# Performance work log

Measured on AMD Instinct MI355X. Metric: run time of the kernel, lower is better.

Reference implementation:

```python
import math
import jax, jax.numpy as jnp
import numpy as np

H, KV, D = 16, 4, 128          # num_heads, num_kv_heads, head_dim
HID = 2048                      # hidden_size
ROPE_BASE = 1e6
EPS = 1e-6


def setup_inputs() -> dict:
    key = jax.random.key(0)
    ks = jax.random.split(key, 3)
    B, S = 2, 2048
    s = 0.02
    return {
        "x": jax.random.normal(ks[0], (B, S, HID), jnp.float32),
        "w_qkv": jax.random.normal(ks[1], (2 * H * D + 2 * KV * D, HID), jnp.float32) * s,
        "w_o": jax.random.normal(ks[2], (HID, H * D), jnp.float32) * s,
        "q_norm_w": jnp.ones((D,), jnp.float32),
        "q_norm_b": jnp.zeros((D,), jnp.float32),
        "k_norm_w": jnp.ones((D,), jnp.float32),
        "k_norm_b": jnp.zeros((D,), jnp.float32),
    }


def _layernorm(x, w, b):
    mu = jnp.mean(x, axis=-1, keepdims=True)
    xc = x - mu
    var = jnp.mean(xc * xc, axis=-1, keepdims=True)
    return xc * jax.lax.rsqrt(var + EPS) * w + b


def _rope(x, cos, sin):
    # x: [B, h, S, D]; cos/sin: [S, D/2]; interleaved real/imag pairs
    xr, xi = x[..., 0::2], x[..., 1::2]
    c, s = cos[None, None], sin[None, None]
    out = jnp.stack([xr * c - xi * s, xr * s + xi * c], axis=-1)
    return out.reshape(x.shape)


def reference(x, w_qkv, w_o, q_norm_w, q_norm_b, k_norm_w, k_norm_b):
    B, S, _ = x.shape
    qkv = x @ w_qkv.T                                  # [B,S,2*H*D+2*KV*D]
    qg, k, v = jnp.split(qkv, [2 * H * D, 2 * H * D + KV * D], axis=-1)
    q, gate = jnp.split(qg, 2, axis=-1)                # [B,S,H*D] each

    q = q.reshape(B, S, H, D).transpose(0, 2, 1, 3)    # [B,H,S,D]
    k = k.reshape(B, S, KV, D).transpose(0, 2, 1, 3)   # [B,KV,S,D]
    v = v.reshape(B, S, KV, D).transpose(0, 2, 1, 3)

    q = _layernorm(q, q_norm_w, q_norm_b)
    k = _layernorm(k, k_norm_w, k_norm_b)

    inv = 1.0 / (ROPE_BASE ** (jnp.arange(0, D, 2, dtype=jnp.float32) / D))
    freqs = jnp.outer(jnp.arange(S, dtype=jnp.float32), inv)  # [S, D/2]
    cos, sin = jnp.cos(freqs), jnp.sin(freqs)
    q = _rope(q, cos, sin)
    k = _rope(k, cos, sin)

    rep = H // KV
    k = jnp.repeat(k, rep, axis=1)                     # [B,H,S,D]
    v = jnp.repeat(v, rep, axis=1)

    scores = jnp.einsum('bhqd,bhkd->bhqk', q, k) / math.sqrt(D)
    causal = jnp.tril(jnp.ones((S, S), bool))
    scores = jnp.where(causal[None, None], scores, -jnp.inf)
    attn = jax.nn.softmax(scores, axis=-1)
    out = jnp.einsum('bhqk,bhkd->bhqd', attn, v)
    out = out.transpose(0, 2, 1, 3).reshape(B, S, H * D)
    out = out * jax.nn.sigmoid(gate)
    return out @ w_o.T
```

## Files before the change

kernel.cpp:

```cpp
#include <hip/hip_runtime.h>
#include <hip/hip_bf16.h>

typedef __bf16 bf16_t;
typedef __bf16 bf16x2 __attribute__((ext_vector_type(2)));
typedef __bf16 bf16x4v __attribute__((ext_vector_type(4)));
typedef __bf16 bf16x8 __attribute__((ext_vector_type(8)));
typedef float f32x4 __attribute__((ext_vector_type(4)));

#define LOG2E 1.4426950408889634f
#define QSCALE (0.08838834764831843f * 1.4426950408889634f)

__global__ __launch_bounds__(256) void cvt_all(const float* __restrict__ x, bf16_t* __restrict__ xb,
                                               const float* __restrict__ wq, bf16_t* __restrict__ wqb,
                                               const float* __restrict__ wo, bf16_t* __restrict__ wob) {
  int i = blockIdx.x * 256 + threadIdx.x;
  const float* in; bf16_t* out; int idx;
  if (i < 2097152)      { in = x;  out = xb;  idx = i; }
  else if (i < 4718592) { in = wq; out = wqb; idx = i - 2097152; }
  else                  { in = wo; out = wob; idx = i - 4718592; }
  float4 v = ((const float4*)in)[idx];
  bf16x4v o;
  o[0] = (__bf16)v.x; o[1] = (__bf16)v.y; o[2] = (__bf16)v.z; o[3] = (__bf16)v.w;
  *(bf16x4v*)(out + (size_t)idx * 4) = o;
}

__global__ __launch_bounds__(256) void rope_tables(float* __restrict__ cosT,
                                                   float* __restrict__ sinT) {
  int idx = blockIdx.x * 256 + threadIdx.x;
  int s = idx >> 6, i = idx & 63;
  float inv = __builtin_amdgcn_exp2f(-(float)i * (19.931568569324174f / 64.0f));
  float f = (float)s * inv;
  cosT[idx] = cosf(f);
  sinT[idx] = sinf(f);
}

template<int MI, int NI, typename OT>
__global__ __launch_bounds__(512) void gemm8p(const bf16_t* __restrict__ A,
                                              const bf16_t* __restrict__ B,
                                              OT* __restrict__ C,
                                              int M, int N, int K) {
  constexpr int BM = MI * 32;
  constexpr int BN = NI * 64;
  constexpr int NA = BM / 64;
  constexpr int NB = BN / 64;
  constexpr int ST = NA + NB;

  __shared__ bf16_t LA[2][BM * 64];
  __shared__ bf16_t LB[2][BN * 64];

  int nb = N / BN;
  int cpx = gridDim.x >> 3;
  int bid = blockIdx.x;
  int swz = (bid & 7) * cpx + (bid >> 3);
  int bm = swz / nb, bn = swz % nb;
  int m0 = bm * BM, n0 = bn * BN;
  int tid = threadIdx.x, lane = tid & 63, wv = tid >> 6;
  int wr = wv >> 2, wc = wv & 3, lr = lane & 15, g = lane >> 4;
  int T = K >> 6;

  auto stageI = [&](int kt, int bi, int s) {
    int k0 = kt << 6;
    if (s < NA) {
      int c = s * 512 + tid;
      int row = c >> 3, lc = (c & 7) ^ (row & 7);
      __builtin_amdgcn_global_load_lds(
          (const __attribute__((address_space(1))) void*)(A + (size_t)(m0 + row) * K + k0 + lc * 8),
          (__attribute__((address_space(3))) void*)&LA[bi][(s * 512 + wv * 64) * 8], 16, 0, 0);
    } else {
      int c = (s - NA) * 512 + tid;
      int row = c >> 3, lc = (c & 7) ^ (row & 7);
      __builtin_amdgcn_global_load_lds(
          (const __attribute__((address_space(1))) void*)(B + (size_t)(n0 + row) * K + k0 + lc * 8),
          (__attribute__((address_space(3))) void*)&LB[bi][((s - NA) * 512 + wv * 64) * 8], 16, 0, 0);
    }
  };

  f32x4 acc[MI][NI];
#pragma unroll
  for (int i = 0; i < MI; i++)
#pragma unroll
    for (int j = 0; j < NI; j++)
#pragma unroll
      for (int r = 0; r < 4; r++) acc[i][j][r] = 0.f;

#pragma unroll
  for (int s = 0; s < ST; s++) stageI(0, 0, s);
  asm volatile("s_waitcnt vmcnt(0)" ::: "memory");
  __builtin_amdgcn_s_barrier();
  asm volatile("" ::: "memory");

  int ofk0 = ((0 + g) ^ (lr & 7)) << 3;
  int ofk1 = ((4 + g) ^ (lr & 7)) << 3;
  int offA = (wr * (MI * 16) + lr) * 64;
  int offB = (wc * (NI * 16) + lr) * 64;

  for (int t = 0; t < T; t++) {
    int bi = t & 1, bo = bi ^ 1;
    const bf16_t* la = LA[bi];
    const bf16_t* lb = LB[bi];
    bool pre = (t + 1 < T);
    if (pre) {
#pragma unroll
      for (int s = 0; s < ST; s++) stageI(t + 1, bo, s);
    }

    bf16x8 bq0[NI], bq1[NI];
#pragma unroll
    for (int ni = 0; ni < NI; ni++) bq0[ni] = *(const bf16x8*)&lb[offB + ni * 1024 + ofk0];
#pragma unroll
    for (int ni = 0; ni < NI; ni++) bq1[ni] = *(const bf16x8*)&lb[offB + ni * 1024 + ofk1];
#pragma unroll
    for (int q = 0; q < MI / 4; q++) {
      bf16x8 af0[4], af1[4];
#pragma unroll
      for (int i = 0; i < 4; i++)
        af0[i] = *(const bf16x8*)&la[offA + (q * 4 + i) * 1024 + ofk0];
#pragma unroll
      for (int i = 0; i < 4; i++)
#pragma unroll
        for (int ni = 0; ni < NI; ni++)
          acc[q * 4 + i][ni] =
              __builtin_amdgcn_mfma_f32_16x16x32_bf16(af0[i], bq0[ni], acc[q * 4 + i][ni], 0, 0, 0);
#pragma unroll
      for (int i = 0; i < 4; i++)
        af1[i] = *(const bf16x8*)&la[offA + (q * 4 + i) * 1024 + ofk1];
#pragma unroll
      for (int i = 0; i < 4; i++)
#pragma unroll
        for (int ni = 0; ni < NI; ni++)
          acc[q * 4 + i][ni] =
              __builtin_amdgcn_mfma_f32_16x16x32_bf16(af1[i], bq1[ni], acc[q * 4 + i][ni], 0, 0, 0);
    }

    if (pre) {
      asm volatile("s_waitcnt vmcnt(0) lgkmcnt(0)" ::: "memory");
      __builtin_amdgcn_s_barrier();
      asm volatile("" ::: "memory");
    }
  }

#pragma unroll
  for (int mi = 0; mi < MI; mi++)
#pragma unroll
    for (int ni = 0; ni < NI; ni++) {
      int m = m0 + wr * (MI * 16) + mi * 16 + g * 4;
      int n = n0 + wc * (NI * 16) + ni * 16 + lr;
#pragma unroll
      for (int r = 0; r < 4; r++) C[(size_t)(m + r) * N + n] = (OT)acc[mi][ni][r];
    }
}

__global__ __launch_bounds__(256) void ln_rope(const bf16_t* __restrict__ qkv,
                                               const float* __restrict__ qw, const float* __restrict__ qb,
                                               const float* __restrict__ kw, const float* __restrict__ kb,
                                               const float* __restrict__ cosT, const float* __restrict__ sinT,
                                               bf16_t* __restrict__ Qr, bf16_t* __restrict__ Kr) {
  int row = blockIdx.x;
  int b = row >> 11, s = row & 2047;
  int tid = threadIdx.x, gi = tid >> 4, li = tid & 15;
  const bf16_t* base = qkv + (size_t)row * 5120;
  float4 c4 = *(const float4*)(cosT + (s << 6) + (li << 2));
  float4 s4 = *(const float4*)(sinT + (s << 6) + (li << 2));
#pragma unroll
  for (int it = 0; it < 2; it++) {
    int head;
    if (it == 0) head = gi;
    else { if (gi >= 4) break; head = 16 + gi; }
    bool isq = (it == 0);
    int off = isq ? (head << 7) : (4096 + ((head - 16) << 7));
    bf16x8 xv = *(const bf16x8*)(base + off + (li << 3));
    float xf[8];
#pragma unroll
    for (int j = 0; j < 8; j++) xf[j] = (float)xv[j];
    float sum = 0.f;
#pragma unroll
    for (int j = 0; j < 8; j++) sum += xf[j];
#pragma unroll
    for (int m = 1; m < 16; m <<= 1) sum += __shfl_xor(sum, m);
    float mu = sum * 0.0078125f;
    float vs = 0.f;
#pragma unroll
    for (int j = 0; j < 8; j++) { xf[j] -= mu; vs += xf[j] * xf[j]; }
#pragma unroll
    for (int m = 1; m < 16; m <<= 1) vs += __shfl_xor(vs, m);
    float rs = rsqrtf(vs * 0.0078125f + 1e-6f);
    const float* w = isq ? qw : kw;
    const float* bb = isq ? qb : kb;
    float4 w0 = *(const float4*)(w + (li << 3));
    float4 w1 = *(const float4*)(w + (li << 3) + 4);
    float4 b0 = *(const float4*)(bb + (li << 3));
    float4 b1 = *(const float4*)(bb + (li << 3) + 4);
    float y[8];
    y[0] = xf[0] * rs * w0.x + b0.x; y[1] = xf[1] * rs * w0.y + b0.y;
    y[2] = xf[2] * rs * w0.z + b0.z; y[3] = xf[3] * rs * w0.w + b0.w;
    y[4] = xf[4] * rs * w1.x + b1.x; y[5] = xf[5] * rs * w1.y + b1.y;
    y[6] = xf[6] * rs * w1.z + b1.z; y[7] = xf[7] * rs * w1.w + b1.w;
    float cc[4] = { c4.x, c4.y, c4.z, c4.w };
    float ss[4] = { s4.x, s4.y, s4.z, s4.w };
    bf16x8 ov;
#pragma unroll
    for (int p = 0; p < 4; p++) {
      float o0 = y[2 * p] * cc[p] - y[2 * p + 1] * ss[p];
      float o1 = y[2 * p] * ss[p] + y[2 * p + 1] * cc[p];
      if (isq) { o0 *= QSCALE; o1 *= QSCALE; }
      ov[2 * p] = (__bf16)o0; ov[2 * p + 1] = (__bf16)o1;
    }
    size_t dst = isq ? ((((size_t)(b * 16 + head)) * 2048 + s) * 128 + (li << 3))
                     : ((((size_t)(b * 4 + (head - 16))) * 2048 + s) * 128 + (li << 3));
    *(bf16x8*)((isq ? Qr : Kr) + dst) = ov;
  }
}

__global__ __launch_bounds__(256) void vtrans(const bf16_t* __restrict__ qkv,
                                              bf16_t* __restrict__ Vt) {
  int bid = blockIdx.x;
  int sb = bid & 63, kv = (bid >> 6) & 3, b = bid >> 8;
  int s0 = sb << 5;
  __shared__ bf16_t T[128 * 33];
  int tid = threadIdx.x;
#pragma unroll
  for (int i = 0; i < 16; i++) {
    int idx = i * 256 + tid;
    int r = idx >> 7, d = idx & 127;
    T[d * 33 + r] = qkv[((size_t)(b * 2048 + s0 + r)) * 5120 + 4608 + (kv << 7) + d];
  }
  __syncthreads();
#pragma unroll
  for (int j = 0; j < 16; j++) {
    int idx = j * 256 + tid;
    int d = idx >> 5, sc = idx & 31;
    Vt[(((size_t)(b * 4 + kv)) * 128 + d) * 2048 + s0 + sc] = T[d * 33 + sc];
  }
}

__global__ __launch_bounds__(256, 3) void attn(const bf16_t* __restrict__ Qr,
                                               const bf16_t* __restrict__ Kr,
                                               const bf16_t* __restrict__ Vt,
                                               const bf16_t* __restrict__ qkv,
                                               bf16_t* __restrict__ ag) {
  __shared__ bf16_t Ks[2][32 * 128];
  __shared__ bf16_t Vs[2][128 * 32];
  int bid = blockIdx.x;
  int hb = bid & 31;
  int h = hb & 15, b = hb >> 4;
  int pr = bid >> 5;
  int kvh = h >> 2;
  int tid = threadIdx.x, lane = tid & 63, wv = tid >> 6;
  int lr = lane & 15, g = lane >> 4;
  int r0base = ((lr >> 2) << 3) + (lr & 3);

  const bf16_t* Kg = Kr + ((size_t)(b * 4 + kvh)) * 2048 * 128;
  const bf16_t* Vg = Vt + ((size_t)(b * 4 + kvh)) * 128 * 2048;

  auto stage = [&](int buf, int kv0) {
#pragma unroll
    for (int i = 0; i < 2; i++) {
      int c = i * 256 + tid;
      int row = c >> 4, lc = (c & 15) ^ (row & 15);
      __builtin_amdgcn_global_load_lds(
          (const __attribute__((address_space(1))) void*)(Kg + (size_t)(kv0 + row) * 128 + lc * 8),
          (__attribute__((address_space(3))) void*)&Ks[buf][c * 8], 16, 0, 0);
    }
#pragma unroll
    for (int i = 0; i < 2; i++) {
      int c = i * 256 + tid;
      int d = c >> 2, cv = (c & 3) ^ ((d >> 1) & 3);
      __builtin_amdgcn_global_load_lds(
          (const __attribute__((address_space(1))) void*)(Vg + (size_t)d * 2048 + kv0 + cv * 8),
          (__attribute__((address_space(3))) void*)&Vs[buf][c * 8], 16, 0, 0);
    }
  };

  auto sm = [&](const f32x4& s0, const f32x4& s1, int qrow, int kvabs, bool dia,
                float& mrun, float& lsp, bf16x8& pb, f32x4 (&oac)[8]) {
    float tt[8];
#pragma unroll
    for (int r = 0; r < 4; r++) { tt[r] = s0[r]; tt[4 + r] = s1[r]; }
    if (dia) {
#pragma unroll
      for (int r = 0; r < 4; r++) {
        if (kvabs + r > qrow)     tt[r]     = -1e30f;
        if (kvabs + 4 + r > qrow) tt[4 + r] = -1e30f;
      }
    }
    float lm = fmaxf(fmaxf(fmaxf(tt[0], tt[1]), tt[2]),
                     fmaxf(fmaxf(tt[3], tt[4]), fmaxf(fmaxf(tt[5], tt[6]), tt[7])));
    if (__all(lm <= mrun + 8.f)) {
      float ps = 0.f;
#pragma unroll
      for (int i = 0; i < 8; i++) {
        float pv = __builtin_amdgcn_exp2f(tt[i] - mrun);
        pb[i] = (__bf16)pv; ps += pv;
      }
      lsp += ps;
    } else {
      float pm = lm;
      pm = fmaxf(pm, __shfl_xor(pm, 16));
      pm = fmaxf(pm, __shfl_xor(pm, 32));
      float mnew = fmaxf(mrun, pm);
      float corr = __builtin_amdgcn_exp2f(mrun - mnew);
      float ps = 0.f;
#pragma unroll
      for (int i = 0; i < 8; i++) {
        float pv = __builtin_amdgcn_exp2f(tt[i] - mnew);
        pb[i] = (__bf16)pv; ps += pv;
      }
      lsp = lsp * corr + ps;
      mrun = mnew;
#pragma unroll
      for (int dt = 0; dt < 8; dt++)
#pragma unroll
        for (int r = 0; r < 4; r++) oac[dt][r] *= corr;
    }
  };

  for (int phase = 0; phase < 2; phase++) {
    int qb = phase ? (31 - pr) : pr;
    int qw0 = qb << 6;
    int qw = qw0 + (wv << 4);
    int qrow = qw + lr;
    int qmax = qw + 15;
    int nt = (qb + 1) << 1;

    const bf16_t* Qg = Qr + (((size_t)(b * 16 + h)) * 2048 + qrow) * 128;
    bf16x8 qf[4];
#pragma unroll
    for (int ds = 0; ds < 4; ds++) qf[ds] = *(const bf16x8*)(Qg + ds * 32 + g * 8);

    f32x4 oa[8];
#pragma unroll
    for (int i = 0; i < 8; i++)
#pragma unroll
      for (int r = 0; r < 4; r++) oa[i][r] = 0.f;
    float mrun = -1e30f, lsp = 0.f;

    stage(0, 0);
    asm volatile("s_waitcnt vmcnt(0)" ::: "memory");
    __builtin_amdgcn_s_barrier();
    asm volatile("" ::: "memory");
    for (int t = 0; t < nt; t++) {
      int cur = t & 1;
      if (t + 1 < nt) stage(cur ^ 1, (t + 1) << 5);
      int kvb = t << 5;
      if (kvb <= qmax) {
        const bf16_t* kb = Ks[cur];
        const bf16_t* vb = Vs[cur];
        int ra = r0base, rb2 = r0base + 4;
        bf16x8 a0[4], a1[4];
#pragma unroll
        for (int ds = 0; ds < 4; ds++) {
          a0[ds] = *(const bf16x8*)&kb[ra * 128 + (((ds * 4 + g) ^ (ra & 15)) << 3)];
          a1[ds] = *(const bf16x8*)&kb[rb2 * 128 + (((ds * 4 + g) ^ (rb2 & 15)) << 3)];
        }
        f32x4 s0, s1;
#pragma unroll
        for (int r = 0; r < 4; r++) { s0[r] = 0.f; s1[r] = 0.f; }
        __builtin_amdgcn_s_setprio(1);
#pragma unroll
        for (int ds = 0; ds < 4; ds++) {
          s0 = __builtin_amdgcn_mfma_f32_16x16x32_bf16(a0[ds], qf[ds], s0, 0, 0, 0);
          s1 = __builtin_amdgcn_mfma_f32_16x16x32_bf16(a1[ds], qf[ds], s1, 0, 0, 0);
        }
        __builtin_amdgcn_s_setprio(0);
        int kvabs = kvb + (g << 3);
        bool dia = (kvb + 31 > qw);
        bf16x8 pb;
        sm(s0, s1, qrow, kvabs, dia, mrun, lsp, pb, oa);
        __builtin_amdgcn_s_setprio(1);
#pragma unroll
        for (int dt = 0; dt < 8; dt++) {
          int d = dt * 16 + lr;
          bf16x8 va = *(const bf16x8*)&vb[d * 32 + ((g ^ ((d >> 1) & 3)) << 3)];
          oa[dt] = __builtin_amdgcn_mfma_f32_16x16x32_bf16(va, pb, oa[dt], 0, 0, 0);
        }
        __builtin_amdgcn_s_setprio(0);
      }
      asm volatile("s_waitcnt vmcnt(0) lgkmcnt(0)" ::: "memory");
      __builtin_amdgcn_s_barrier();
      asm volatile("" ::: "memory");
    }

    float ls = lsp + __shfl_xor(lsp, 16);
    ls += __shfl_xor(ls, 32);
    float invl = __builtin_amdgcn_rcpf(ls);

    size_t ob = ((size_t)b * 2048 + qrow) * 2048 + (h << 7);
    size_t gb = ((size_t)b * 2048 + qrow) * 5120 + 2048 + (h << 7);
#pragma unroll
    for (int dt = 0; dt < 8; dt++) {
      int d = dt * 16 + (g << 2);
      bf16x4v gt = *(const bf16x4v*)(qkv + gb + d);
      bf16x4v o;
      o[0] = (__bf16)(oa[dt][0] * invl * __builtin_amdgcn_rcpf(1.f + __builtin_amdgcn_exp2f(-(float)gt[0] * LOG2E)));
      o[1] = (__bf16)(oa[dt][1] * invl * __builtin_amdgcn_rcpf(1.f + __builtin_amdgcn_exp2f(-(float)gt[1] * LOG2E)));
      o[2] = (__bf16)(oa[dt][2] * invl * __builtin_amdgcn_rcpf(1.f + __builtin_amdgcn_exp2f(-(float)gt[2] * LOG2E)));
      o[3] = (__bf16)(oa[dt][3] * invl * __builtin_amdgcn_rcpf(1.f + __builtin_amdgcn_exp2f(-(float)gt[3] * LOG2E)));
      *(bf16x4v*)(ag + ob + d) = o;
    }
  }
}

extern "C" void kernel_launch(void* const* d_in, const int* in_sizes, int n_in,
                              void* d_out, int out_size, void* d_ws, size_t ws_size,
                              hipStream_t stream) {
  const float* x    = (const float*)d_in[0];
  const float* wqkv = (const float*)d_in[1];
  const float* wo   = (const float*)d_in[2];
  const float* qnw  = (const float*)d_in[3];
  const float* qnb  = (const float*)d_in[4];
  const float* knw  = (const float*)d_in[5];
  const float* knb  = (const float*)d_in[6];
  float* out = (float*)d_out;

  char* p = (char*)d_ws;
  bf16_t* xb  = (bf16_t*)p;
  bf16_t* ag  = xb;
  p += (size_t)16777216;
  bf16_t* wqb = (bf16_t*)p;
  bf16_t* Qr  = wqb;
  p += (size_t)20971520;
  bf16_t* wob = (bf16_t*)p; p += (size_t)8388608;
  bf16_t* qkv = (bf16_t*)p; p += (size_t)41943040;
  bf16_t* Kr  = (bf16_t*)p; p += (size_t)4194304;
  bf16_t* Vt  = (bf16_t*)p; p += (size_t)4194304;
  float* cosT = (float*)p;  p += (size_t)524288;
  float* sinT = (float*)p;  p += (size_t)524288;

  cvt_all<<<22528, 256, 0, stream>>>(x, xb, wqkv, wqb, wo, wob);
  rope_tables<<<512, 256, 0, stream>>>(cosT, sinT);

  gemm8p<8, 5, bf16_t><<<256, 512, 0, stream>>>(xb, wqb, qkv, 4096, 5120, 2048);

  ln_rope<<<4096, 256, 0, stream>>>(qkv, qnw, qnb, knw, knb, cosT, sinT, Qr, Kr);
  vtrans<<<512, 256, 0, stream>>>(qkv, Vt);

  attn<<<512, 256, 0, stream>>>(Qr, Kr, Vt, qkv, ag);

  gemm8p<4, 4, float><<<256, 512, 0, stream>>>(ag, wob, out, 4096, 2048, 2048);
}
```

Measured before the change: 232.7 us.

## Shrink GEMM K-tile to 32 and use smaller 128-row tiles for higher occupancy

Result: slower. 282.4 us (+21.4%).

```diff
diff --git a/kernel.cpp b/kernel.cpp
--- a/kernel.cpp
+++ b/kernel.cpp
@@ -34,19 +34,19 @@
   sinT[idx] = sinf(f);
 }
 
-template<int MI, int NI, typename OT>
-__global__ __launch_bounds__(512) void gemm8p(const bf16_t* __restrict__ A,
-                                              const bf16_t* __restrict__ B,
-                                              OT* __restrict__ C,
-                                              int M, int N, int K) {
-  constexpr int BM = MI * 32;
+template<int NI, typename OT>
+__global__ __launch_bounds__(512, 4) void gemmk(const bf16_t* __restrict__ A,
+                                                const bf16_t* __restrict__ B,
+                                                OT* __restrict__ C,
+                                                int M, int N, int K) {
+  constexpr int BM = 128;
   constexpr int BN = NI * 64;
-  constexpr int NA = BM / 64;
-  constexpr int NB = BN / 64;
+  constexpr int NA = 1;
+  constexpr int NB = BN / 128;
   constexpr int ST = NA + NB;
 
-  __shared__ bf16_t LA[2][BM * 64];
-  __shared__ bf16_t LB[2][BN * 64];
+  __shared__ bf16_t LA[2][BM * 32];
+  __shared__ bf16_t LB[2][BN * 32];
 
   int nb = N / BN;
   int cpx = gridDim.x >> 3;
@@ -56,28 +56,28 @@
   int m0 = bm * BM, n0 = bn * BN;
   int tid = threadIdx.x, lane = tid & 63, wv = tid >> 6;
   int wr = wv >> 2, wc = wv & 3, lr = lane & 15, g = lane >> 4;
-  int T = K >> 6;
+  int T = K >> 5;
 
   auto stageI = [&](int kt, int bi, int s) {
-    int k0 = kt << 6;
+    int k0 = kt << 5;
     if (s < NA) {
-      int c = s * 512 + tid;
-      int row = c >> 3, lc = (c & 7) ^ (row & 7);
+      int c = tid;
+      int row = c >> 2, lc = (c & 3) ^ (row & 3);
       __builtin_amdgcn_global_load_lds(
           (const __attribute__((address_space(1))) void*)(A + (size_t)(m0 + row) * K + k0 + lc * 8),
-          (__attribute__((address_space(3))) void*)&LA[bi][(s * 512 + wv * 64) * 8], 16, 0, 0);
+          (__attribute__((address_space(3))) void*)&LA[bi][wv * 512], 16, 0, 0);
     } else {
       int c = (s - NA) * 512 + tid;
-      int row = c >> 3, lc = (c & 7) ^ (row & 7);
+      int row = c >> 2, lc = (c & 3) ^ (row & 3);
       __builtin_amdgcn_global_load_lds(
           (const __attribute__((address_space(1))) void*)(B + (size_t)(n0 + row) * K + k0 + lc * 8),
           (__attribute__((address_space(3))) void*)&LB[bi][((s - NA) * 512 + wv * 64) * 8], 16, 0, 0);
     }
   };
 
-  f32x4 acc[MI][NI];
-#pragma unroll
-  for (int i = 0; i < MI; i++)
+  f32x4 acc[4][NI];
+#pragma unroll
+  for (int i = 0; i < 4; i++)
 #pragma unroll
     for (int j = 0; j < NI; j++)
 #pragma unroll
@@ -89,10 +89,9 @@
   __builtin_amdgcn_s_barrier();
   asm volatile("" ::: "memory");
 
-  int ofk0 = ((0 + g) ^ (lr & 7)) << 3;
-  int ofk1 = ((4 + g) ^ (lr & 7)) << 3;
-  int offA = (wr * (MI * 16) + lr) * 64;
-  int offB = (wc * (NI * 16) + lr) * 64;
+  int ofk = (g ^ (lr & 3)) << 3;
+  int offA = (wr * 64 + lr) * 32;
+  int offB = (wc * (NI * 16) + lr) * 32;
 
   for (int t = 0; t < T; t++) {
     int bi = t & 1, bo = bi ^ 1;
@@ -104,33 +103,16 @@
       for (int s = 0; s < ST; s++) stageI(t + 1, bo, s);
     }
 
-    bf16x8 bq0[NI], bq1[NI];
-#pragma unroll
-    for (int ni = 0; ni < NI; ni++) bq0[ni] = *(const bf16x8*)&lb[offB + ni * 1024 + ofk0];
-#pragma unroll
-    for (int ni = 0; ni < NI; ni++) bq1[ni] = *(const bf16x8*)&lb[offB + ni * 1024 + ofk1];
-#pragma unroll
-    for (int q = 0; q < MI / 4; q++) {
-      bf16x8 af0[4], af1[4];
-#pragma unroll
-      for (int i = 0; i < 4; i++)
-        af0[i] = *(const bf16x8*)&la[offA + (q * 4 + i) * 1024 + ofk0];
-#pragma unroll
-      for (int i = 0; i < 4; i++)
-#pragma unroll
-        for (int ni = 0; ni < NI; ni++)
-          acc[q * 4 + i][ni] =
-              __builtin_amdgcn_mfma_f32_16x16x32_bf16(af0[i], bq0[ni], acc[q * 4 + i][ni], 0, 0, 0);
-#pragma unroll
-      for (int i = 0; i < 4; i++)
-        af1[i] = *(const bf16x8*)&la[offA + (q * 4 + i) * 1024 + ofk1];
-#pragma unroll
-      for (int i = 0; i < 4; i++)
-#pragma unroll
-        for (int ni = 0; ni < NI; ni++)
-          acc[q * 4 + i][ni] =
-              __builtin_amdgcn_mfma_f32_16x16x32_bf16(af1[i], bq1[ni], acc[q * 4 + i][ni], 0, 0, 0);
-    }
+    bf16x8 bq[NI], af[4];
+#pragma unroll
+    for (int ni = 0; ni < NI; ni++) bq[ni] = *(const bf16x8*)&lb[offB + ni * 512 + ofk];
+#pragma unroll
+    for (int i = 0; i < 4; i++)     af[i]  = *(const bf16x8*)&la[offA + i * 512 + ofk];
+#pragma unroll
+    for (int i = 0; i < 4; i++)
+#pragma unroll
+      for (int ni = 0; ni < NI; ni++)
+        acc[i][ni] = __builtin_amdgcn_mfma_f32_16x16x32_bf16(af[i], bq[ni], acc[i][ni], 0, 0, 0);
 
     if (pre) {
       asm volatile("s_waitcnt vmcnt(0) lgkmcnt(0)" ::: "memory");
@@ -140,10 +122,10 @@
   }
 
 #pragma unroll
-  for (int mi = 0; mi < MI; mi++)
+  for (int mi = 0; mi < 4; mi++)
 #pragma unroll
     for (int ni = 0; ni < NI; ni++) {
-      int m = m0 + wr * (MI * 16) + mi * 16 + g * 4;
+      int m = m0 + wr * 64 + mi * 16 + g * 4;
       int n = n0 + wc * (NI * 16) + ni * 16 + lr;
 #pragma unroll
       for (int r = 0; r < 4; r++) C[(size_t)(m + r) * N + n] = (OT)acc[mi][ni][r];
@@ -429,12 +411,12 @@
   cvt_all<<<22528, 256, 0, stream>>>(x, xb, wqkv, wqb, wo, wob);
   rope_tables<<<512, 256, 0, stream>>>(cosT, sinT);
 
-  gemm8p<8, 5, bf16_t><<<256, 512, 0, stream>>>(xb, wqb, qkv, 4096, 5120, 2048);
+  gemmk<4, bf16_t><<<640, 512, 0, stream>>>(xb, wqb, qkv, 4096, 5120, 2048);
 
   ln_rope<<<4096, 256, 0, stream>>>(qkv, qnw, qnb, knw, knb, cosT, sinT, Qr, Kr);
   vtrans<<<512, 256, 0, stream>>>(qkv, Vt);
 
   attn<<<512, 256, 0, stream>>>(Qr, Kr, Vt, qkv, ag);
 
-  gemm8p<4, 4, float><<<256, 512, 0, stream>>>(ag, wob, out, 4096, 2048, 2048);
-}
+  gemmk<4, float><<<256, 512, 0, stream>>>(ag, wob, out, 4096, 2048, 2048);
+}
```

## Process 128 query rows per attention block with two 16-row tiles per wave

Applied to the files above, without the earlier changes.

New measurement: 275.6 us. 1.18x slower.

```diff
diff --git a/kernel.cpp b/kernel.cpp
--- a/kernel.cpp
+++ b/kernel.cpp
@@ -233,24 +233,37 @@
   }
 }
 
-__global__ __launch_bounds__(256, 3) void attn(const bf16_t* __restrict__ Qr,
-                                               const bf16_t* __restrict__ Kr,
-                                               const bf16_t* __restrict__ Vt,
-                                               const bf16_t* __restrict__ qkv,
-                                               bf16_t* __restrict__ ag) {
+__global__ __launch_bounds__(256) void attn(const bf16_t* __restrict__ Qr,
+                                            const bf16_t* __restrict__ Kr,
+                                            const bf16_t* __restrict__ Vt,
+                                            const bf16_t* __restrict__ qkv,
+                                            bf16_t* __restrict__ ag) {
   __shared__ bf16_t Ks[2][32 * 128];
   __shared__ bf16_t Vs[2][128 * 32];
   int bid = blockIdx.x;
   int hb = bid & 31;
   int h = hb & 15, b = hb >> 4;
-  int pr = bid >> 5;
+  int qc = 15 - (bid >> 5);
   int kvh = h >> 2;
   int tid = threadIdx.x, lane = tid & 63, wv = tid >> 6;
   int lr = lane & 15, g = lane >> 4;
   int r0base = ((lr >> 2) << 3) + (lr & 3);
 
+  int qw = (qc << 7) + (wv << 5);
+  int qrow0 = qw + lr, qrow1 = qrow0 + 16;
+  int qmax = qw + 31;
+  int nt = (qc + 1) << 2;
+
   const bf16_t* Kg = Kr + ((size_t)(b * 4 + kvh)) * 2048 * 128;
   const bf16_t* Vg = Vt + ((size_t)(b * 4 + kvh)) * 128 * 2048;
+
+  const bf16_t* Qg = Qr + (((size_t)(b * 16 + h)) * 2048 + qrow0) * 128;
+  bf16x8 qf0[4], qf1[4];
+#pragma unroll
+  for (int ds = 0; ds < 4; ds++) {
+    qf0[ds] = *(const bf16x8*)(Qg + ds * 32 + g * 8);
+    qf1[ds] = *(const bf16x8*)(Qg + 16 * 128 + ds * 32 + g * 8);
+  }
 
   auto stage = [&](int buf, int kv0) {
 #pragma unroll
@@ -314,89 +327,89 @@
     }
   };
 
-  for (int phase = 0; phase < 2; phase++) {
-    int qb = phase ? (31 - pr) : pr;
-    int qw0 = qb << 6;
-    int qw = qw0 + (wv << 4);
-    int qrow = qw + lr;
-    int qmax = qw + 15;
-    int nt = (qb + 1) << 1;
-
-    const bf16_t* Qg = Qr + (((size_t)(b * 16 + h)) * 2048 + qrow) * 128;
-    bf16x8 qf[4];
-#pragma unroll
-    for (int ds = 0; ds < 4; ds++) qf[ds] = *(const bf16x8*)(Qg + ds * 32 + g * 8);
-
-    f32x4 oa[8];
-#pragma unroll
-    for (int i = 0; i < 8; i++)
-#pragma unroll
-      for (int r = 0; r < 4; r++) oa[i][r] = 0.f;
-    float mrun = -1e30f, lsp = 0.f;
-
-    stage(0, 0);
-    asm volatile("s_waitcnt vmcnt(0)" ::: "memory");
+  f32x4 oa0[8], oa1[8];
+#pragma unroll
+  for (int i = 0; i < 8; i++)
+#pragma unroll
+    for (int r = 0; r < 4; r++) { oa0[i][r] = 0.f; oa1[i][r] = 0.f; }
+  float mrun0 = -1e30f, mrun1 = -1e30f, lsp0 = 0.f, lsp1 = 0.f;
+
+  stage(0, 0);
+  asm volatile("s_waitcnt vmcnt(0)" ::: "memory");
+  __builtin_amdgcn_s_barrier();
+  asm volatile("" ::: "memory");
+  for (int t = 0; t < nt; t++) {
+    int cur = t & 1;
+    if (t + 1 < nt) stage(cur ^ 1, (t + 1) << 5);
+    int kvb = t << 5;
+    if (kvb <= qmax) {
+      const bf16_t* kb = Ks[cur];
+      const bf16_t* vb = Vs[cur];
+      int ra = r0base, rb2 = r0base + 4;
+      bf16x8 a0[4], a1[4];
+#pragma unroll
+      for (int ds = 0; ds < 4; ds++) {
+        a0[ds] = *(const bf16x8*)&kb[ra * 128 + (((ds * 4 + g) ^ (ra & 15)) << 3)];
+        a1[ds] = *(const bf16x8*)&kb[rb2 * 128 + (((ds * 4 + g) ^ (rb2 & 15)) << 3)];
+      }
+      f32x4 s00, s10, s01, s11;
+#pragma unroll
+      for (int r = 0; r < 4; r++) { s00[r] = 0.f; s10[r] = 0.f; s01[r] = 0.f; s11[r] = 0.f; }
+      __builtin_amdgcn_s_setprio(1);
+#pragma unroll
+      for (int ds = 0; ds < 4; ds++) {
+        s00 = __builtin_amdgcn_mfma_f32_16x16x32_bf16(a0[ds], qf0[ds], s00, 0, 0, 0);
+        s10 = __builtin_amdgcn_mfma_f32_16x16x32_bf16(a1[ds], qf0[ds], s10, 0, 0, 0);
+        s01 = __builtin_amdgcn_mfma_f32_16x16x32_bf16(a0[ds], qf1[ds], s01, 0, 0, 0);
+        s11 = __builtin_amdgcn_mfma_f32_16x16x32_bf16(a1[ds], qf1[ds], s11, 0, 0, 0);
+      }
+      __builtin_amdgcn_s_setprio(0);
+      int kvabs = kvb + (g << 3);
+      bool dia = (kvb + 31 > qw);
+      bf16x8 pb0, pb1;
+      sm(s00, s10, qrow0, kvabs, dia, mrun0, lsp0, pb0, oa0);
+      sm(s01, s11, qrow1, kvabs, dia, mrun1, lsp1, pb1, oa1);
+      __builtin_amdgcn_s_setprio(1);
+#pragma unroll
+      for (int dt = 0; dt < 8; dt++) {
+        int d = dt * 16 + lr;
+        bf16x8 va = *(const bf16x8*)&vb[d * 32 + ((g ^ ((d >> 1) & 3)) << 3)];
+        oa0[dt] = __builtin_amdgcn_mfma_f32_16x16x32_bf16(va, pb0, oa0[dt], 0, 0, 0);
+        oa1[dt] = __builtin_amdgcn_mfma_f32_16x16x32_bf16(va, pb1, oa1[dt], 0, 0, 0);
+      }
+      __builtin_amdgcn_s_setprio(0);
+    }
+    asm volatile("s_waitcnt vmcnt(0) lgkmcnt(0)" ::: "memory");
     __builtin_amdgcn_s_barrier();
     asm volatile("" ::: "memory");
-    for (int t = 0; t < nt; t++) {
-      int cur = t & 1;
-      if (t + 1 < nt) stage(cur ^ 1, (t + 1) << 5);
-      int kvb = t << 5;
-      if (kvb <= qmax) {
-        const bf16_t* kb = Ks[cur];
-        const bf16_t* vb = Vs[cur];
-        int ra = r0base, rb2 = r0base + 4;
-        bf16x8 a0[4], a1[4];
-#pragma unroll
-        for (int ds = 0; ds < 4; ds++) {
-          a0[ds] = *(const bf16x8*)&kb[ra * 128 + (((ds * 4 + g) ^ (ra & 15)) << 3)];
-          a1[ds] = *(const bf16x8*)&kb[rb2 * 128 + (((ds * 4 + g) ^ (rb2 & 15)) << 3)];
-        }
-        f32x4 s0, s1;
-#pragma unroll
-        for (int r = 0; r < 4; r++) { s0[r] = 0.f; s1[r] = 0.f; }
-        __builtin_amdgcn_s_setprio(1);
-#pragma unroll
-        for (int ds = 0; ds < 4; ds++) {
-          s0 = __builtin_amdgcn_mfma_f32_16x16x32_bf16(a0[ds], qf[ds], s0, 0, 0, 0);
-          s1 = __builtin_amdgcn_mfma_f32_16x16x32_bf16(a1[ds], qf[ds], s1, 0, 0, 0);
-        }
-        __builtin_amdgcn_s_setprio(0);
-        int kvabs = kvb + (g << 3);
-        bool dia = (kvb + 31 > qw);
-        bf16x8 pb;
-        sm(s0, s1, qrow, kvabs, dia, mrun, lsp, pb, oa);
-        __builtin_amdgcn_s_setprio(1);
-#pragma unroll
-        for (int dt = 0; dt < 8; dt++) {
-          int d = dt * 16 + lr;
-          bf16x8 va = *(const bf16x8*)&vb[d * 32 + ((g ^ ((d >> 1) & 3)) << 3)];
-          oa[dt] = __builtin_amdgcn_mfma_f32_16x16x32_bf16(va, pb, oa[dt], 0, 0, 0);
-        }
-        __builtin_amdgcn_s_setprio(0);
-      }
-      asm volatile("s_waitcnt vmcnt(0) lgkmcnt(0)" ::: "memory");
-      __builtin_amdgcn_s_barrier();
-      asm volatile("" ::: "memory");
-    }
-
-    float ls = lsp + __shfl_xor(lsp, 16);
-    ls += __shfl_xor(ls, 32);
-    float invl = __builtin_amdgcn_rcpf(ls);
-
-    size_t ob = ((size_t)b * 2048 + qrow) * 2048 + (h << 7);
-    size_t gb = ((size_t)b * 2048 + qrow) * 5120 + 2048 + (h << 7);
-#pragma unroll
-    for (int dt = 0; dt < 8; dt++) {
-      int d = dt * 16 + (g << 2);
-      bf16x4v gt = *(const bf16x4v*)(qkv + gb + d);
-      bf16x4v o;
-      o[0] = (__bf16)(oa[dt][0] * invl * __builtin_amdgcn_rcpf(1.f + __builtin_amdgcn_exp2f(-(float)gt[0] * LOG2E)));
-      o[1] = (__bf16)(oa[dt][1] * invl * __builtin_amdgcn_rcpf(1.f + __builtin_amdgcn_exp2f(-(float)gt[1] * LOG2E)));
-      o[2] = (__bf16)(oa[dt][2] * invl * __builtin_amdgcn_rcpf(1.f + __builtin_amdgcn_exp2f(-(float)gt[2] * LOG2E)));
-      o[3] = (__bf16)(oa[dt][3] * invl * __builtin_amdgcn_rcpf(1.f + __builtin_amdgcn_exp2f(-(float)gt[3] * LOG2E)));
-      *(bf16x4v*)(ag + ob + d) = o;
-    }
+  }
+
+  float ls0 = lsp0 + __shfl_xor(lsp0, 16);
+  ls0 += __shfl_xor(ls0, 32);
+  float ls1 = lsp1 + __shfl_xor(lsp1, 16);
+  ls1 += __shfl_xor(ls1, 32);
+  float invl0 = __builtin_amdgcn_rcpf(ls0);
+  float invl1 = __builtin_amdgcn_rcpf(ls1);
+
+  size_t ob0 = ((size_t)b * 2048 + qrow0) * 2048 + (h << 7);
+  size_t gb0 = ((size_t)b * 2048 + qrow0) * 5120 + 2048 + (h << 7);
+  size_t ob1 = ((size_t)b * 2048 + qrow1) * 2048 + (h << 7);
+  size_t gb1 = ((size_t)b * 2048 + qrow1) * 5120 + 2048 + (h << 7);
+#pragma unroll
+  for (int dt = 0; dt < 8; dt++) {
+    int d = dt * 16 + (g << 2);
+    bf16x4v gt0 = *(const bf16x4v*)(qkv + gb0 + d);
+    bf16x4v gt1 = *(const bf16x4v*)(qkv + gb1 + d);
+    bf16x4v o0, o1;
+#pragma unroll
+    for (int r = 0; r < 4; r++) {
+      o0[r] = (__bf16)(oa0[dt][r] * invl0 *
+                       __builtin_amdgcn_rcpf(1.f + __builtin_amdgcn_exp2f(-(float)gt0[r] * LOG2E)));
+      o1[r] = (__bf16)(oa1[dt][r] * invl1 *
+                       __builtin_amdgcn_rcpf(1.f + __builtin_amdgcn_exp2f(-(float)gt1[r] * LOG2E)));
+    }
+    *(bf16x4v*)(ag + ob0 + d) = o0;
+    *(bf16x4v*)(ag + ob1 + d) = o1;
   }
 }
 
```

## Fuse RoPE table generation into conversion kernel and reorder GEMM LDS fragment loads

Applied to the files above, without the earlier changes.

Measured after the change: 231.5 us. About the same (-0.5%).

```diff
diff --git a/kernel.cpp b/kernel.cpp
--- a/kernel.cpp
+++ b/kernel.cpp
@@ -12,26 +12,26 @@
 
 __global__ __launch_bounds__(256) void cvt_all(const float* __restrict__ x, bf16_t* __restrict__ xb,
                                                const float* __restrict__ wq, bf16_t* __restrict__ wqb,
-                                               const float* __restrict__ wo, bf16_t* __restrict__ wob) {
+                                               const float* __restrict__ wo, bf16_t* __restrict__ wob,
+                                               float* __restrict__ cosT, float* __restrict__ sinT) {
   int i = blockIdx.x * 256 + threadIdx.x;
-  const float* in; bf16_t* out; int idx;
-  if (i < 2097152)      { in = x;  out = xb;  idx = i; }
-  else if (i < 4718592) { in = wq; out = wqb; idx = i - 2097152; }
-  else                  { in = wo; out = wob; idx = i - 4718592; }
-  float4 v = ((const float4*)in)[idx];
-  bf16x4v o;
-  o[0] = (__bf16)v.x; o[1] = (__bf16)v.y; o[2] = (__bf16)v.z; o[3] = (__bf16)v.w;
-  *(bf16x4v*)(out + (size_t)idx * 4) = o;
-}
-
-__global__ __launch_bounds__(256) void rope_tables(float* __restrict__ cosT,
-                                                   float* __restrict__ sinT) {
-  int idx = blockIdx.x * 256 + threadIdx.x;
-  int s = idx >> 6, i = idx & 63;
-  float inv = __builtin_amdgcn_exp2f(-(float)i * (19.931568569324174f / 64.0f));
-  float f = (float)s * inv;
-  cosT[idx] = cosf(f);
-  sinT[idx] = sinf(f);
+  if (i < 5767168) {
+    const float* in; bf16_t* out; int idx;
+    if (i < 2097152)      { in = x;  out = xb;  idx = i; }
+    else if (i < 4718592) { in = wq; out = wqb; idx = i - 2097152; }
+    else                  { in = wo; out = wob; idx = i - 4718592; }
+    float4 v = ((const float4*)in)[idx];
+    bf16x4v o;
+    o[0] = (__bf16)v.x; o[1] = (__bf16)v.y; o[2] = (__bf16)v.z; o[3] = (__bf16)v.w;
+    *(bf16x4v*)(out + (size_t)idx * 4) = o;
+  } else {
+    int idx = i - 5767168;
+    int s = idx >> 6, fi = idx & 63;
+    float inv = __builtin_amdgcn_exp2f(-(float)fi * (19.931568569324174f / 64.0f));
+    float f = (float)s * inv;
+    cosT[idx] = cosf(f);
+    sinT[idx] = sinf(f);
+  }
 }
 
 template<int MI, int NI, typename OT>
@@ -44,6 +44,7 @@
   constexpr int NA = BM / 64;
   constexpr int NB = BN / 64;
   constexpr int ST = NA + NB;
+  static_assert(MI == 8 || MI == 4, "banked phases assume MI in {4,8}");
 
   __shared__ bf16_t LA[2][BM * 64];
   __shared__ bf16_t LB[2][BN * 64];
@@ -104,32 +105,56 @@
       for (int s = 0; s < ST; s++) stageI(t + 1, bo, s);
     }
 
-    bf16x8 bq0[NI], bq1[NI];
+    bf16x8 bq0[NI], bq1[NI], afA[4], afB[4];
 #pragma unroll
     for (int ni = 0; ni < NI; ni++) bq0[ni] = *(const bf16x8*)&lb[offB + ni * 1024 + ofk0];
 #pragma unroll
-    for (int ni = 0; ni < NI; ni++) bq1[ni] = *(const bf16x8*)&lb[offB + ni * 1024 + ofk1];
-#pragma unroll
-    for (int q = 0; q < MI / 4; q++) {
-      bf16x8 af0[4], af1[4];
-#pragma unroll
-      for (int i = 0; i < 4; i++)
-        af0[i] = *(const bf16x8*)&la[offA + (q * 4 + i) * 1024 + ofk0];
-#pragma unroll
-      for (int i = 0; i < 4; i++)
-#pragma unroll
-        for (int ni = 0; ni < NI; ni++)
-          acc[q * 4 + i][ni] =
-              __builtin_amdgcn_mfma_f32_16x16x32_bf16(af0[i], bq0[ni], acc[q * 4 + i][ni], 0, 0, 0);
-#pragma unroll
-      for (int i = 0; i < 4; i++)
-        af1[i] = *(const bf16x8*)&la[offA + (q * 4 + i) * 1024 + ofk1];
-#pragma unroll
-      for (int i = 0; i < 4; i++)
-#pragma unroll
-        for (int ni = 0; ni < NI; ni++)
-          acc[q * 4 + i][ni] =
-              __builtin_amdgcn_mfma_f32_16x16x32_bf16(af1[i], bq1[ni], acc[q * 4 + i][ni], 0, 0, 0);
+    for (int i = 0; i < 4; i++) afA[i] = *(const bf16x8*)&la[offA + i * 1024 + ofk0];
+
+    if constexpr (MI == 8) {
+#pragma unroll
+      for (int i = 0; i < 4; i++) afB[i] = *(const bf16x8*)&la[offA + (4 + i) * 1024 + ofk0];
+#pragma unroll
+      for (int i = 0; i < 4; i++)
+#pragma unroll
+        for (int ni = 0; ni < NI; ni++)
+          acc[i][ni] = __builtin_amdgcn_mfma_f32_16x16x32_bf16(afA[i], bq0[ni], acc[i][ni], 0, 0, 0);
+#pragma unroll
+      for (int i = 0; i < 4; i++) afA[i] = *(const bf16x8*)&la[offA + i * 1024 + ofk1];
+#pragma unroll
+      for (int ni = 0; ni < NI; ni++) bq1[ni] = *(const bf16x8*)&lb[offB + ni * 1024 + ofk1];
+#pragma unroll
+      for (int i = 0; i < 4; i++)
+#pragma unroll
+        for (int ni = 0; ni < NI; ni++)
+          acc[4 + i][ni] = __builtin_amdgcn_mfma_f32_16x16x32_bf16(afB[i], bq0[ni], acc[4 + i][ni], 0, 0, 0);
+#pragma unroll
+      for (int i = 0; i < 4; i++) afB[i] = *(const bf16x8*)&la[offA + (4 + i) * 1024 + ofk1];
+#pragma unroll
+      for (int i = 0; i < 4; i++)
+#pragma unroll
+        for (int ni = 0; ni < NI; ni++)
+          acc[i][ni] = __builtin_amdgcn_mfma_f32_16x16x32_bf16(afA[i], bq1[ni], acc[i][ni], 0, 0, 0);
+#pragma unroll
+      for (int i = 0; i < 4; i++)
+#pragma unroll
+        for (int ni = 0; ni < NI; ni++)
+          acc[4 + i][ni] = __builtin_amdgcn_mfma_f32_16x16x32_bf16(afB[i], bq1[ni], acc[4 + i][ni], 0, 0, 0);
+    } else {
+#pragma unroll
+      for (int i = 0; i < 4; i++) afB[i] = *(const bf16x8*)&la[offA + i * 1024 + ofk1];
+#pragma unroll
+      for (int ni = 0; ni < NI; ni++) bq1[ni] = *(const bf16x8*)&lb[offB + ni * 1024 + ofk1];
+#pragma unroll
+      for (int i = 0; i < 4; i++)
+#pragma unroll
+        for (int ni = 0; ni < NI; ni++)
+          acc[i][ni] = __builtin_amdgcn_mfma_f32_16x16x32_bf16(afA[i], bq0[ni], acc[i][ni], 0, 0, 0);
+#pragma unroll
+      for (int i = 0; i < 4; i++)
+#pragma unroll
+        for (int ni = 0; ni < NI; ni++)
+          acc[i][ni] = __builtin_amdgcn_mfma_f32_16x16x32_bf16(afB[i], bq1[ni], acc[i][ni], 0, 0, 0);
     }
 
     if (pre) {
@@ -391,10 +416,10 @@
       int d = dt * 16 + (g << 2);
       bf16x4v gt = *(const bf16x4v*)(qkv + gb + d);
       bf16x4v o;
-      o[0] = (__bf16)(oa[dt][0] * invl * __builtin_amdgcn_rcpf(1.f + __builtin_amdgcn_exp2f(-(float)gt[0] * LOG2E)));
-      o[1] = (__bf16)(oa[dt][1] * invl * __builtin_amdgcn_rcpf(1.f + __builtin_amdgcn_exp2f(-(float)gt[1] * LOG2E)));
-      o[2] = (__bf16)(oa[dt][2] * invl * __builtin_amdgcn_rcpf(1.f + __builtin_amdgcn_exp2f(-(float)gt[2] * LOG2E)));
-      o[3] = (__bf16)(oa[dt][3] * invl * __builtin_amdgcn_rcpf(1.f + __builtin_amdgcn_exp2f(-(float)gt[3] * LOG2E)));
+#pragma unroll
+      for (int r = 0; r < 4; r++)
+        o[r] = (__bf16)(oa[dt][r] * invl *
+                        __builtin_amdgcn_rcpf(1.f + __builtin_amdgcn_exp2f(-(float)gt[r] * LOG2E)));
       *(bf16x4v*)(ag + ob + d) = o;
     }
   }
@@ -426,8 +451,7 @@
   float* cosT = (float*)p;  p += (size_t)524288;
   float* sinT = (float*)p;  p += (size_t)524288;
 
-  cvt_all<<<22528, 256, 0, stream>>>(x, xb, wqkv, wqb, wo, wob);
-  rope_tables<<<512, 256, 0, stream>>>(cosT, sinT);
+  cvt_all<<<23040, 256, 0, stream>>>(x, xb, wqkv, wqb, wo, wob, cosT, sinT);
 
   gemm8p<8, 5, bf16_t><<<256, 512, 0, stream>>>(xb, wqb, qkv, 4096, 5120, 2048);
 
```
